# Optimization experiments

Hardware: AMD Instinct MI355X
Metric: run time of the kernel (lower is better)

## Reference

```python
import jax, jax.numpy as jnp
import numpy as np

PATCH = (9, 7, 5, 3)
DIM = 64
HEAD_DIM = 64
HEADS = 8
HIDDEN = 8
DEPTH = 4
SCALE = (HEAD_DIM / HEADS) ** (-0.5)  # per-head dim = 8
EPS = 1e-5


def setup_inputs() -> dict:
    key = jax.random.key(0)
    ks = jax.random.split(key, 8)
    B = 4096
    x = jax.random.normal(ks[0], (B, PATCH[0] * PATCH[0], DIM), dtype=jnp.float32)
    w_qkv = jax.random.normal(ks[1], (DEPTH, DIM, 3 * HEAD_DIM), dtype=jnp.float32) * 0.05
    b_qkv = jnp.zeros((DEPTH, 3 * HEAD_DIM), dtype=jnp.float32)
    w_o = jax.random.normal(ks[2], (DEPTH, HEAD_DIM, DIM), dtype=jnp.float32) * 0.05
    b_o = jnp.zeros((DEPTH, DIM), dtype=jnp.float32)
    ln1_g = jnp.ones((DEPTH, DIM), dtype=jnp.float32)
    ln1_b = jnp.zeros((DEPTH, DIM), dtype=jnp.float32)
    ln2_g = jnp.ones((DEPTH, DIM), dtype=jnp.float32)
    ln2_b = jnp.zeros((DEPTH, DIM), dtype=jnp.float32)
    w1 = jax.random.normal(ks[3], (DEPTH, DIM, HIDDEN), dtype=jnp.float32) * 0.05
    b1 = jnp.zeros((DEPTH, HIDDEN), dtype=jnp.float32)
    w2 = jax.random.normal(ks[4], (DEPTH, HIDDEN, DIM), dtype=jnp.float32) * 0.05
    b2 = jnp.zeros((DEPTH, DIM), dtype=jnp.float32)
    return {"x": x, "w_qkv": w_qkv, "b_qkv": b_qkv, "w_o": w_o, "b_o": b_o,
            "ln1_g": ln1_g, "ln1_b": ln1_b, "ln2_g": ln2_g, "ln2_b": ln2_b,
            "w1": w1, "b1": b1, "w2": w2, "b2": b2}


def _layernorm(x, g, b):
    m = jnp.mean(x, axis=-1, keepdims=True)
    v = jnp.mean(jnp.square(x - m), axis=-1, keepdims=True)
    return (x - m) * jax.lax.rsqrt(v + EPS) * g + b


def reference(x, w_qkv, b_qkv, w_o, b_o, ln1_g, ln1_b, ln2_g, ln2_b, w1, b1, w2, b2):
    B = x.shape[0]
    for i in range(DEPTH):
        n = x.shape[1]
        # --- attention block (Residual(Layernorm(Encoder))) ---
        y = _layernorm(x, ln1_g[i], ln1_b[i])
        qkv = y @ w_qkv[i] + b_qkv[i]                       # [B, n, 3*HEAD_DIM]
        q, k, v = jnp.split(qkv, 3, axis=-1)
        dh = HEAD_DIM // HEADS                              # 8
        q = q.reshape(B, n, HEADS, dh)
        k = k.reshape(B, n, HEADS, dh)
        v = v.reshape(B, n, HEADS, dh)
        dots = jnp.einsum('bihd,bjhd->bhij', q, k) * SCALE  # [B, H, n, n]
        attn = jax.nn.softmax(dots, axis=-1)
        out = jnp.einsum('bhij,bjhd->bihd', attn, v).reshape(B, n, HEAD_DIM)
        out = out @ w_o[i] + b_o[i]
        x = x + out                                         # dropout = identity (eval)
        # --- feedforward block ---
        y = _layernorm(x, ln2_g[i], ln2_b[i])
        h = jax.nn.gelu(y @ w1[i] + b1[i], approximate=False)
        x = x + h @ w2[i] + b2[i]
        # --- spatial pooling / rearrange ---
        p = PATCH[i]
        xg = x.reshape(B, p, p, DIM)                        # 'b (h w) d -> b h w d'
        if i != DEPTH - 1:
            xg = xg[:, 1:-1, 1:-1, :]                       # crop pool_size=1
            x = xg.reshape(B, (p - 2) * (p - 2), DIM)
        else:
            x = jnp.transpose(xg, (0, 3, 1, 2))             # 'b h w d -> b d h w'
    return x  # [B, 64, 3, 3]
```

## Files before the change

kernel.cpp:

```cpp
#include <hip/hip_runtime.h>
#include <hip/hip_bf16.h>
#include <math.h>

#define NT 512

typedef __attribute__((ext_vector_type(8))) short short8v;
typedef __attribute__((ext_vector_type(4))) short short4v;
typedef __attribute__((ext_vector_type(4))) float f32x4;
typedef __attribute__((ext_vector_type(2))) unsigned uint2v;
typedef __attribute__((ext_vector_type(4))) unsigned uint4v;

__device__ __forceinline__ unsigned short f2bf(float x) {
    unsigned u = __float_as_uint(x);
    unsigned r = ((u >> 16) & 1u) + 0x7FFFu;
    return (unsigned short)((u + r) >> 16);
}
__device__ __forceinline__ unsigned pk2(float a, float b) {
    __hip_bfloat162 h = __float22bfloat162_rn(make_float2(a, b));
    unsigned r;
    __builtin_memcpy(&r, &h, sizeof(r));
    return r;
}
__device__ __forceinline__ short bf1(float a) {
    __hip_bfloat16 h = __float2bfloat16(a);
    short r;
    __builtin_memcpy(&r, &h, sizeof(r));
    return r;
}
__device__ __forceinline__ float exp2fast(float x) {
#if __has_builtin(__builtin_amdgcn_exp2f)
    return __builtin_amdgcn_exp2f(x);
#else
    return exp2f(x);
#endif
}
__device__ __forceinline__ float gelu_f(float x) {
    float x3 = x * x * x;
    float e = exp2fast(-2.3022079f * x - 0.1029432f * x3);
    return x / (1.0f + e);
}
__device__ __forceinline__ f32x4 mfma32(short8v a, short8v b, f32x4 c) {
    return __builtin_amdgcn_mfma_f32_16x16x32_bf16(a, b, c, 0, 0, 0);
}

template<int M>
__device__ __forceinline__ float sum_tree(const f32x4* a) {
    float p[M];
    #pragma unroll
    for (int i = 0; i < M; ++i)
        p[i] = (a[i][0] + a[i][1]) + (a[i][2] + a[i][3]);
    #pragma unroll
    for (int s = 1; s < M; s *= 2)
        #pragma unroll
        for (int i = 0; i + s < M; i += 2 * s) p[i] += p[i + s];
    return p[0];
}
template<int M>
__device__ __forceinline__ void stats_tree(const f32x4* v, float& s1o, float& s2o) {
    float a[M], b[M];
    #pragma unroll
    for (int i = 0; i < M; ++i) {
        a[i] = (v[i][0] + v[i][1]) + (v[i][2] + v[i][3]);
        float q0 = v[i][0] * v[i][0], q1 = v[i][1] * v[i][1];
        float q2 = v[i][2] * v[i][2], q3 = v[i][3] * v[i][3];
        b[i] = (q0 + q1) + (q2 + q3);
    }
    #pragma unroll
    for (int s = 1; s < M; s *= 2)
        #pragma unroll
        for (int i = 0; i + s < M; i += 2 * s) { a[i] += a[i + s]; b[i] += b[i + s]; }
    s1o = a[0]; s2o = b[0];
}

#define WS_WO 49152
#define WS_W1 65536
#define WS_W2 69632
#define WS_TOT 71680

__global__ __launch_bounds__(256) void prep_kernel(
    const float* __restrict__ w_qkv, const float* __restrict__ w_o,
    const float* __restrict__ w1, const float* __restrict__ w2,
    short* __restrict__ ws)
{
    int idx = blockIdx.x * 256 + threadIdx.x;
    if (idx < WS_WO) {
        int l = idx / 12288, r = idx % 12288, c = r >> 6, d = r & 63;
        ws[idx] = (short)f2bf(w_qkv[l * 12288 + d * 192 + c]);
    } else if (idx < WS_W1) {
        int k = idx - WS_WO; int l = k / 4096, r = k % 4096, c = r >> 6, d = r & 63;
        ws[idx] = (short)f2bf(w_o[l * 4096 + d * 64 + c]);
    } else if (idx < WS_W2) {
        int k = idx - WS_W1; int l = k / 1024, r = k % 1024, j = r >> 6, d = r & 63;
        ws[idx] = (j < 8) ? (short)f2bf(w1[l * 512 + d * 8 + j]) : (short)0;
    } else if (idx < WS_TOT) {
        int k = idx - WS_W2; int l = k / 512, r = k % 512, c = r >> 3, j = r & 7;
        ws[idx] = (short)f2bf(w2[l * 512 + j * 64 + c]);
    }
}

template<int N, int P, int L, bool FIRST, bool LAST>
__device__ __forceinline__ void layer_fn(
    float* __restrict__ xs, short* __restrict__ y, short* __restrict__ vb,
    short* __restrict__ qbf, short* __restrict__ kbf,
    const short* __restrict__ ws,
    const float* __restrict__ b_qkv, const float* __restrict__ b_o,
    const float* __restrict__ ln1_g, const float* __restrict__ ln1_b,
    const float* __restrict__ ln2_g, const float* __restrict__ ln2_b,
    const float* __restrict__ b1,    const float* __restrict__ b2,
    float* __restrict__ out, int b, int t)
{
    constexpr int Mt = (N + 15) / 16;
    constexpr float SCL2E = 0.51010905835f;
    const int wv = t >> 6, l = t & 63, lr = l & 15, lq = l >> 4;
    short8v zero8 = {};
    f32x4 zero4 = {0.f, 0.f, 0.f, 0.f};

    if (FIRST) {
        if (t < 64 * Mt) {
            const int token = t >> 2, part = t & 3, d0 = part * 16;
            short* yrow = y + token * 72 + d0;
            if (token < N) {
                const int row = (token / P + L) * 9 + token % P + L;
                const float* xr = xs + row * 68 + d0;
                f32x4 v[4];
                #pragma unroll
                for (int k = 0; k < 4; ++k) v[k] = *(const f32x4*)(xr + 4 * k);
                float s1, s2;
                stats_tree<4>(v, s1, s2);
                s1 += __shfl_xor(s1, 1); s2 += __shfl_xor(s2, 1);
                s1 += __shfl_xor(s1, 2); s2 += __shfl_xor(s2, 2);
                const float m = s1 * 0.015625f;
                const float r = rsqrtf(s2 * 0.015625f - m * m + 1e-5f);
                uint4v w0, w1v;
                #pragma unroll
                for (int k = 0; k < 4; ++k) {
                    f32x4 g  = *(const f32x4*)&ln1_g[L * 64 + d0 + 4 * k];
                    f32x4 bb = *(const f32x4*)&ln1_b[L * 64 + d0 + 4 * k];
                    unsigned p0 = pk2((v[k][0]-m)*r*g[0]+bb[0], (v[k][1]-m)*r*g[1]+bb[1]);
                    unsigned p1 = pk2((v[k][2]-m)*r*g[2]+bb[2], (v[k][3]-m)*r*g[3]+bb[3]);
                    if (k == 0) { w0.x = p0; w0.y = p1; }
                    else if (k == 1) { w0.z = p0; w0.w = p1; }
                    else if (k == 2) { w1v.x = p0; w1v.y = p1; }
                    else { w1v.z = p0; w1v.w = p1; }
                }
                *(uint4v*)yrow = w0;
                *(uint4v*)(yrow + 8) = w1v;
            } else {
                uint4v z = {};
                *(uint4v*)yrow = z;
                *(uint4v*)(yrow + 8) = z;
            }
        }
        __syncthreads();
    }

    {
        const short* wqL = ws + L * 12288;
        for (int u = wv; u < Mt * 12; u += 8) {
            const int mt = u / 12, ct = u - mt * 12;
            const short* yr = &y[(16 * mt + lr) * 72 + lq * 8];
            short8v y0 = *(const short8v*)yr, y1 = *(const short8v*)(yr + 32);
            const short* wr = &wqL[(16 * ct + lr) * 64 + lq * 8];
            short8v w0 = *(const short8v*)wr, w1 = *(const short8v*)(wr + 32);
            if (ct < 8) {
                f32x4 acc = mfma32(w0, y0, zero4);
                acc = mfma32(w1, y1, acc);
                f32x4 bq = *(const f32x4*)&b_qkv[L * 192 + 16 * ct + lq * 4];
                const int i = 16 * mt + lr;
                if (ct < 4) {
                    unsigned p0 = pk2((acc[0]+bq[0])*SCL2E, (acc[1]+bq[1])*SCL2E);
                    unsigned p1 = pk2((acc[2]+bq[2])*SCL2E, (acc[3]+bq[3])*SCL2E);
                    unsigned* dst = (unsigned*)&qbf[i * 72 + 16 * ct + lq * 4];
                    dst[0] = p0; dst[1] = p1;
                } else {
                    unsigned p0 = pk2(acc[0]+bq[0], acc[1]+bq[1]);
                    unsigned p1 = pk2(acc[2]+bq[2], acc[3]+bq[3]);
                    unsigned* dst = (unsigned*)&kbf[i * 72 + 16 * (ct - 4) + lq * 4];
                    dst[0] = p0; dst[1] = p1;
                }
            } else {
                f32x4 acc = mfma32(y0, w0, zero4);
                acc = mfma32(y1, w1, acc);
                const int cv = 16 * (ct - 8) + lr;
                const float bias = b_qkv[L * 192 + 128 + cv];
                unsigned p0 = pk2(acc[0]+bias, acc[1]+bias);
                unsigned p1 = pk2(acc[2]+bias, acc[3]+bias);
                unsigned* dst = (unsigned*)&vb[cv * 104 + 16 * mt + lq * 4];
                dst[0] = p0; dst[1] = p1;
            }
        }
    }
    __syncthreads();

    {
        const int h = wv, hh = wv >> 1;
        short8v kf[Mt];
        #pragma unroll
        for (int jt = 0; jt < Mt; ++jt)
            kf[jt] = (l < 16) ? *(const short8v*)&kbf[(16 * jt + lr) * 72 + h * 8] : zero8;
#if __has_builtin(__builtin_amdgcn_mfma_f32_16x16x16bf16_1k)
        short4v vf[Mt];
        #pragma unroll
        for (int jt = 0; jt < Mt; ++jt)
            vf[jt] = *(const short4v*)&vb[(16 * hh + lr) * 104 + 16 * jt + lq * 4];
#else
        constexpr int KS2 = (Mt + 1) / 2;
        short8v vf8[KS2];
        #pragma unroll
        for (int ks = 0; ks < KS2; ++ks)
            vf8[ks] = *(const short8v*)&vb[(16 * hh + lr) * 104 + 32 * ks + lq * 8];
#endif
        for (int mt = 0; mt < Mt; ++mt) {
            short8v bq = (l < 16) ? *(const short8v*)&qbf[(16 * mt + lr) * 72 + h * 8] : zero8;
            f32x4 acc[Mt];
            #pragma unroll
            for (int jt = 0; jt < Mt; ++jt) acc[jt] = mfma32(kf[jt], bq, zero4);
            #pragma unroll
            for (int jt = 0; jt < Mt; ++jt) {
                #pragma unroll
                for (int rg = 0; rg < 4; ++rg) {
                    float e = exp2fast(acc[jt][rg]);
                    if (jt == Mt - 1) {
                        const int j = 16 * jt + lq * 4 + rg;
                        e = (j < N) ? e : 0.f;
                    }
                    acc[jt][rg] = e;
                }
            }
            float psum = sum_tree<Mt>(acc);
            float den = psum + __shfl_xor(psum, 16);
            den += __shfl_xor(den, 32);
            const float dinv = 1.0f / den;
            unsigned pkk[Mt][2];
            #pragma unroll
            for (int jt = 0; jt < Mt; ++jt) {
                pkk[jt][0] = pk2(acc[jt][0], acc[jt][1]);
                pkk[jt][1] = pk2(acc[jt][2], acc[jt][3]);
            }
            f32x4 po0 = zero4, po1 = zero4;
#if __has_builtin(__builtin_amdgcn_mfma_f32_16x16x16bf16_1k)
            #pragma unroll
            for (int jt = 0; jt < Mt; ++jt) {
                uint2v pw; pw.x = pkk[jt][0]; pw.y = pkk[jt][1];
                short4v bv = __builtin_bit_cast(short4v, pw);
                if (jt & 1) po1 = __builtin_amdgcn_mfma_f32_16x16x16bf16_1k(vf[jt], bv, po1, 0, 0, 0);
                else        po0 = __builtin_amdgcn_mfma_f32_16x16x16bf16_1k(vf[jt], bv, po0, 0, 0, 0);
            }
#else
            #pragma unroll
            for (int ks = 0; ks < KS2; ++ks) {
                const int t1ok = (2 * ks + 1) < Mt;
                unsigned pA0 = pkk[2 * ks][0], pA1 = pkk[2 * ks][1];
                unsigned pB0 = t1ok ? pkk[2 * ks + 1][0] : 0u;
                unsigned pB1 = t1ok ? pkk[2 * ks + 1][1] : 0u;
                int i01 = ((((lq & 1) * 2) * 16) + lr) * 4;
                int i23 = ((((lq & 1) * 2 + 1) * 16) + lr) * 4;
                unsigned w0a = (unsigned)__builtin_amdgcn_ds_bpermute(i01, (int)pA0);
                unsigned w0b = (unsigned)__builtin_amdgcn_ds_bpermute(i01, (int)pB0);
                unsigned w1a = (unsigned)__builtin_amdgcn_ds_bpermute(i01, (int)pA1);
                unsigned w1b = (unsigned)__builtin_amdgcn_ds_bpermute(i01, (int)pB1);
                unsigned w2a = (unsigned)__builtin_amdgcn_ds_bpermute(i23, (int)pA0);
                unsigned w2b = (unsigned)__builtin_amdgcn_ds_bpermute(i23, (int)pB0);
                unsigned w3a = (unsigned)__builtin_amdgcn_ds_bpermute(i23, (int)pA1);
                unsigned w3b = (unsigned)__builtin_amdgcn_ds_bpermute(i23, (int)pB1);
                uint4v wv4;
                wv4.x = (lq >> 1) ? w0b : w0a;
                wv4.y = (lq >> 1) ? w1b : w1a;
                wv4.z = (lq >> 1) ? w2b : w2a;
                wv4.w = (lq >> 1) ? w3b : w3a;
                short8v bv = __builtin_bit_cast(short8v, wv4);
                po0 = mfma32(vf8[ks], bv, po0);
            }
#endif
            if ((lq >> 1) == (h & 1)) {
                const int i = 16 * mt + lr;
                if (i < N) {
                    unsigned q0 = pk2((po0[0]+po1[0])*dinv, (po0[1]+po1[1])*dinv);
                    unsigned q1 = pk2((po0[2]+po1[2])*dinv, (po0[3]+po1[3])*dinv);
                    unsigned* dst = (unsigned*)&y[i * 72 + h * 8 + (lq & 1) * 4];
                    dst[0] = q0; dst[1] = q1;
                }
            }
        }
    }
    __syncthreads();

    {
        short* hb = qbf;
        if (wv < Mt) {
            const int mt = wv;
            const int i = 16 * mt + lr;
            const bool iok = (i < N);
            const int xrow = iok ? (i / P + L) * 9 + (i % P) + L : 0;
            float* xp = xs + xrow * 68;
            const short* yr = &y[i * 72 + lq * 8];
            short8v y0 = *(const short8v*)yr;
            short8v y1 = *(const short8v*)(yr + 32);
            const short* woL = ws + WS_WO + L * 4096;
            f32x4 xv[4];
            #pragma unroll
            for (int ct = 0; ct < 4; ++ct) {
                const short* wr = &woL[(16 * ct + lr) * 64 + lq * 8];
                f32x4 acc = mfma32(*(const short8v*)wr, y0, zero4);
                acc = mfma32(*(const short8v*)(wr + 32), y1, acc);
                f32x4 bo = *(const f32x4*)&b_o[L * 64 + 16 * ct + 4 * lq];
                f32x4 xc = zero4;
                if (iok) xc = *(const f32x4*)(xp + 16 * ct + 4 * lq);
                #pragma unroll
                for (int rg = 0; rg < 4; ++rg) xc[rg] += acc[rg] + bo[rg];
                xv[ct] = xc;
            }
            float s1, s2;
            stats_tree<4>(xv, s1, s2);
            s1 += __shfl_xor(s1, 16); s2 += __shfl_xor(s2, 16);
            s1 += __shfl_xor(s1, 32); s2 += __shfl_xor(s2, 32);
            const float m = s1 * 0.015625f;
            const float r = rsqrtf(s2 * 0.015625f - m * m + 1e-5f);
            unsigned* ybw = (unsigned*)&y[i * 72];
            #pragma unroll
            for (int ct = 0; ct < 4; ++ct) {
                f32x4 g  = *(const f32x4*)&ln2_g[L * 64 + 16 * ct + 4 * lq];
                f32x4 bb = *(const f32x4*)&ln2_b[L * 64 + 16 * ct + 4 * lq];
                ybw[8 * ct + 2 * lq]     = pk2((xv[ct][0]-m)*r*g[0]+bb[0],
                                               (xv[ct][1]-m)*r*g[1]+bb[1]);
                ybw[8 * ct + 2 * lq + 1] = pk2((xv[ct][2]-m)*r*g[2]+bb[2],
                                               (xv[ct][3]-m)*r*g[3]+bb[3]);
            }
            uint4v ua0 = *(const uint4v*)(ybw + 4 * lq);
            uint4v ua1 = *(const uint4v*)(ybw + 16 + 4 * lq);
            const short* w1L = ws + WS_W1 + L * 1024;
            short8v a10 = __builtin_bit_cast(short8v, ua0);
            short8v a11 = __builtin_bit_cast(short8v, ua1);
            short8v b10 = *(const short8v*)&w1L[lr * 64 + lq * 8];
            short8v b11 = *(const short8v*)&w1L[lr * 64 + lq * 8 + 32];
            f32x4 hA = mfma32(a10, b10, zero4);
            hA = mfma32(a11, b11, hA);
            if (lr < 8) {
                const float bg = b1[L * 8 + lr];
                #pragma unroll
                for (int rg = 0; rg < 4; ++rg)
                    hb[(16 * mt + 4 * lq + rg) * 8 + lr] = bf1(gelu_f(hA[rg] + bg));
            }
            short8v hbf = (lq == 0) ? *(const short8v*)&hb[(16 * mt + lr) * 8] : zero8;
            const short* w2L = ws + WS_W2 + L * 512;
            f32x4 xf[4];
            #pragma unroll
            for (int ct = 0; ct < 4; ++ct) {
                short8v a2 = (lq == 0) ? *(const short8v*)&w2L[(16 * ct + lr) * 8] : zero8;
                f32x4 dacc = mfma32(a2, hbf, zero4);
                f32x4 b2v = *(const f32x4*)&b2[L * 64 + 16 * ct + 4 * lq];
                #pragma unroll
                for (int rg = 0; rg < 4; ++rg) xf[ct][rg] = xv[ct][rg] + dacc[rg] + b2v[rg];
                if (iok) *(f32x4*)(xp + 16 * ct + 4 * lq) = xf[ct];
            }
            if (!LAST) {
                float t1, t2;
                stats_tree<4>(xf, t1, t2);
                t1 += __shfl_xor(t1, 16); t2 += __shfl_xor(t2, 16);
                t1 += __shfl_xor(t1, 32); t2 += __shfl_xor(t2, 32);
                const float mn = t1 * 0.015625f;
                const float rn = rsqrtf(t2 * 0.015625f - mn * mn + 1e-5f);
                const int r_ = i / P, c_ = i % P;
                const bool vok = iok && r_ >= 1 && r_ <= P - 2 && c_ >= 1 && c_ <= P - 2;
                if (vok) {
                    const int j = (r_ - 1) * (P - 2) + (c_ - 1);
                    unsigned* yw = (unsigned*)&vb[j * 72];
                    #pragma unroll
                    for (int ct = 0; ct < 4; ++ct) {
                        f32x4 g  = *(const f32x4*)&ln1_g[(L + 1) * 64 + 16 * ct + 4 * lq];
                        f32x4 bb = *(const f32x4*)&ln1_b[(L + 1) * 64 + 16 * ct + 4 * lq];
                        yw[8 * ct + 2 * lq]     = pk2((xf[ct][0]-mn)*rn*g[0]+bb[0],
                                                      (xf[ct][1]-mn)*rn*g[1]+bb[1]);
                        yw[8 * ct + 2 * lq + 1] = pk2((xf[ct][2]-mn)*rn*g[2]+bb[2],
                                                      (xf[ct][3]-mn)*rn*g[3]+bb[3]);
                    }
                }
            }
        } else if (!LAST && wv == Mt) {
            constexpr int Pn = P - 2, Nn = Pn * Pn, Mtn = (Nn + 15) / 16;
            constexpr int PadU = (16 * Mtn - Nn) * 36;
            unsigned* zb = (unsigned*)(vb + Nn * 72);
            for (int z = l; z < PadU; z += 64) zb[z] = 0;
        }
    }
    __syncthreads();

    if (LAST) {
        for (int idx = t; idx < 576; idx += NT) {
            const int d = idx / 9, rc = idx % 9;
            const int row = (rc / 3 + 3) * 9 + rc % 3 + 3;
            out[(size_t)b * 576 + idx] = xs[row * 68 + d];
        }
    }
}

__global__ __launch_bounds__(NT, 4) void vit_kernel(
    const float* __restrict__ x_in, const short* __restrict__ ws,
    const float* __restrict__ b_qkv, const float* __restrict__ b_o,
    const float* __restrict__ ln1_g, const float* __restrict__ ln1_b,
    const float* __restrict__ ln2_g, const float* __restrict__ ln2_b,
    const float* __restrict__ b1,    const float* __restrict__ b2,
    float* __restrict__ out)
{
    __shared__ __align__(16) float xs[81 * 68];
    __shared__ __align__(16) short ybf[96 * 72];
    __shared__ __align__(16) short vbuf[64 * 104];
    __shared__ __align__(16) short qbf[96 * 72];
    __shared__ __align__(16) short kbf[96 * 72];

    const int b = blockIdx.x;
    const int t = threadIdx.x;

    for (int idx = t; idx < 64 * 104; idx += NT) vbuf[idx] = 0;

    const float* xin = x_in + (size_t)b * 5184;
    for (int q4 = t; q4 < 1296; q4 += NT) {
        const int i = q4 >> 4, dq = q4 & 15;
        *(f32x4*)&xs[i * 68 + dq * 4] = *(const f32x4*)&xin[i * 64 + dq * 4];
    }
    __syncthreads();

    layer_fn<81, 9, 0, true,  false>(xs, ybf,  vbuf, qbf, kbf, ws, b_qkv, b_o,
                                     ln1_g, ln1_b, ln2_g, ln2_b, b1, b2, out, b, t);
    layer_fn<49, 7, 1, false, false>(xs, vbuf, ybf,  qbf, kbf, ws, b_qkv, b_o,
                                     ln1_g, ln1_b, ln2_g, ln2_b, b1, b2, out, b, t);
    layer_fn<25, 5, 2, false, false>(xs, ybf,  vbuf, qbf, kbf, ws, b_qkv, b_o,
                                     ln1_g, ln1_b, ln2_g, ln2_b, b1, b2, out, b, t);
    layer_fn<9,  3, 3, false, true >(xs, vbuf, ybf,  qbf, kbf, ws, b_qkv, b_o,
                                     ln1_g, ln1_b, ln2_g, ln2_b, b1, b2, out, b, t);
}

extern "C" void kernel_launch(void* const* d_in, const int* in_sizes, int n_in,
                              void* d_out, int out_size, void* d_ws, size_t ws_size,
                              hipStream_t stream) {
    (void)n_in; (void)out_size; (void)ws_size;
    const float* x     = (const float*)d_in[0];
    const float* w_qkv = (const float*)d_in[1];
    const float* b_qkv = (const float*)d_in[2];
    const float* w_o   = (const float*)d_in[3];
    const float* b_o   = (const float*)d_in[4];
    const float* ln1_g = (const float*)d_in[5];
    const float* ln1_b = (const float*)d_in[6];
    const float* ln2_g = (const float*)d_in[7];
    const float* ln2_b = (const float*)d_in[8];
    const float* w1    = (const float*)d_in[9];
    const float* b1    = (const float*)d_in[10];
    const float* w2    = (const float*)d_in[11];
    const float* b2    = (const float*)d_in[12];
    short* ws = (short*)d_ws;

    prep_kernel<<<dim3((WS_TOT + 255) / 256), dim3(256), 0, stream>>>(w_qkv, w_o, w1, w2, ws);

    int B = in_sizes[0] / (81 * 64);
    vit_kernel<<<dim3(B), dim3(NT), 0, stream>>>(
        x, ws, b_qkv, b_o, ln1_g, ln1_b, ln2_g, ln2_b, b1, b2, (float*)d_out);
}
```

Before: 377.2 us.

## Software-pipeline attention score MFMAs across row tiles and use fast reciprocal

```diff
diff --git a/kernel.cpp b/kernel.cpp
--- a/kernel.cpp
+++ b/kernel.cpp
@@ -34,10 +34,17 @@
     return exp2f(x);
 #endif
 }
+__device__ __forceinline__ float rcpfast(float x) {
+#if __has_builtin(__builtin_amdgcn_rcpf)
+    return __builtin_amdgcn_rcpf(x);
+#else
+    return 1.0f / x;
+#endif
+}
 __device__ __forceinline__ float gelu_f(float x) {
     float x3 = x * x * x;
     float e = exp2fast(-2.3022079f * x - 0.1029432f * x3);
-    return x / (1.0f + e);
+    return x * rcpfast(1.0f + e);
 }
 __device__ __forceinline__ f32x4 mfma32(short8v a, short8v b, f32x4 c) {
     return __builtin_amdgcn_mfma_f32_16x16x32_bf16(a, b, c, 0, 0, 0);
@@ -210,11 +217,12 @@
         for (int ks = 0; ks < KS2; ++ks)
             vf8[ks] = *(const short8v*)&vb[(16 * hh + lr) * 104 + 32 * ks + lq * 8];
 #endif
-        for (int mt = 0; mt < Mt; ++mt) {
-            short8v bq = (l < 16) ? *(const short8v*)&qbf[(16 * mt + lr) * 72 + h * 8] : zero8;
-            f32x4 acc[Mt];
+        auto SCORES = [&](int mt2, f32x4 (&acc)[Mt]) {
+            short8v bq = (l < 16) ? *(const short8v*)&qbf[(16 * mt2 + lr) * 72 + h * 8] : zero8;
             #pragma unroll
             for (int jt = 0; jt < Mt; ++jt) acc[jt] = mfma32(kf[jt], bq, zero4);
+        };
+        auto FINISH = [&](int mt2, f32x4 (&acc)[Mt]) {
             #pragma unroll
             for (int jt = 0; jt < Mt; ++jt) {
                 #pragma unroll
@@ -230,7 +238,7 @@
             float psum = sum_tree<Mt>(acc);
             float den = psum + __shfl_xor(psum, 16);
             den += __shfl_xor(den, 32);
-            const float dinv = 1.0f / den;
+            const float dinv = rcpfast(den);
             unsigned pkk[Mt][2];
             #pragma unroll
             for (int jt = 0; jt < Mt; ++jt) {
@@ -273,13 +281,25 @@
             }
 #endif
             if ((lq >> 1) == (h & 1)) {
-                const int i = 16 * mt + lr;
+                const int i = 16 * mt2 + lr;
                 if (i < N) {
                     unsigned q0 = pk2((po0[0]+po1[0])*dinv, (po0[1]+po1[1])*dinv);
                     unsigned q1 = pk2((po0[2]+po1[2])*dinv, (po0[3]+po1[3])*dinv);
                     unsigned* dst = (unsigned*)&y[i * 72 + h * 8 + (lq & 1) * 4];
                     dst[0] = q0; dst[1] = q1;
                 }
+            }
+        };
+        f32x4 sA[Mt], sB[Mt];
+        SCORES(0, sA);
+        #pragma unroll
+        for (int mt = 0; mt < Mt; ++mt) {
+            if (mt & 1) {
+                if (mt + 1 < Mt) SCORES(mt + 1, sA);
+                FINISH(mt, sB);
+            } else {
+                if (mt + 1 < Mt) SCORES(mt + 1, sB);
+                FINISH(mt, sA);
             }
         }
     }
```

New measurement: 372.7 us (median of 2 runs). Within noise of the previous version (-1.2%).

## Fuse QKV projection into per-head attention with register-resident fragments

Applied to the files above, without the earlier changes.

```diff
diff --git a/kernel.cpp b/kernel.cpp
--- a/kernel.cpp
+++ b/kernel.cpp
@@ -34,27 +34,25 @@
     return exp2f(x);
 #endif
 }
+__device__ __forceinline__ float rcpfast(float x) {
+#if __has_builtin(__builtin_amdgcn_rcpf)
+    return __builtin_amdgcn_rcpf(x);
+#else
+    return 1.0f / x;
+#endif
+}
 __device__ __forceinline__ float gelu_f(float x) {
     float x3 = x * x * x;
     float e = exp2fast(-2.3022079f * x - 0.1029432f * x3);
-    return x / (1.0f + e);
+    return x * rcpfast(1.0f + e);
 }
 __device__ __forceinline__ f32x4 mfma32(short8v a, short8v b, f32x4 c) {
     return __builtin_amdgcn_mfma_f32_16x16x32_bf16(a, b, c, 0, 0, 0);
 }
-
-template<int M>
-__device__ __forceinline__ float sum_tree(const f32x4* a) {
-    float p[M];
-    #pragma unroll
-    for (int i = 0; i < M; ++i)
-        p[i] = (a[i][0] + a[i][1]) + (a[i][2] + a[i][3]);
-    #pragma unroll
-    for (int s = 1; s < M; s *= 2)
-        #pragma unroll
-        for (int i = 0; i + s < M; i += 2 * s) p[i] += p[i + s];
-    return p[0];
-}
+__device__ __forceinline__ f32x4 mfma16(short4v a, short4v b, f32x4 c) {
+    return __builtin_amdgcn_mfma_f32_16x16x16bf16_1k(a, b, c, 0, 0, 0);
+}
+
 template<int M>
 __device__ __forceinline__ void stats_tree(const f32x4* v, float& s1o, float& s2o) {
     float a[M], b[M];
@@ -100,9 +98,8 @@
 
 template<int N, int P, int L, bool FIRST, bool LAST>
 __device__ __forceinline__ void layer_fn(
-    float* __restrict__ xs, short* __restrict__ y, short* __restrict__ vb,
-    short* __restrict__ qbf, short* __restrict__ kbf,
-    const short* __restrict__ ws,
+    float* __restrict__ xs, short* __restrict__ ybuf, short* __restrict__ abuf,
+    short* __restrict__ hb, const short* __restrict__ ws,
     const float* __restrict__ b_qkv, const float* __restrict__ b_o,
     const float* __restrict__ ln1_g, const float* __restrict__ ln1_b,
     const float* __restrict__ ln2_g, const float* __restrict__ ln2_b,
@@ -118,7 +115,7 @@
     if (FIRST) {
         if (t < 64 * Mt) {
             const int token = t >> 2, part = t & 3, d0 = part * 16;
-            short* yrow = y + token * 72 + d0;
+            short* yrow = ybuf + token * 72 + d0;
             if (token < N) {
                 const int row = (token / P + L) * 9 + token % P + L;
                 const float* xr = xs + row * 68 + d0;
@@ -155,129 +152,102 @@
     }
 
     {
+        const int h = wv, a = h & 1, ct = h >> 1;
+        const int srcl = lr + 32 * a + (l & 16);
         const short* wqL = ws + L * 12288;
-        for (int u = wv; u < Mt * 12; u += 8) {
-            const int mt = u / 12, ct = u - mt * 12;
-            const short* yr = &y[(16 * mt + lr) * 72 + lq * 8];
-            short8v y0 = *(const short8v*)yr, y1 = *(const short8v*)(yr + 32);
-            const short* wr = &wqL[(16 * ct + lr) * 64 + lq * 8];
-            short8v w0 = *(const short8v*)wr, w1 = *(const short8v*)(wr + 32);
-            if (ct < 8) {
-                f32x4 acc = mfma32(w0, y0, zero4);
-                acc = mfma32(w1, y1, acc);
-                f32x4 bq = *(const f32x4*)&b_qkv[L * 192 + 16 * ct + lq * 4];
-                const int i = 16 * mt + lr;
-                if (ct < 4) {
-                    unsigned p0 = pk2((acc[0]+bq[0])*SCL2E, (acc[1]+bq[1])*SCL2E);
-                    unsigned p1 = pk2((acc[2]+bq[2])*SCL2E, (acc[3]+bq[3])*SCL2E);
-                    unsigned* dst = (unsigned*)&qbf[i * 72 + 16 * ct + lq * 4];
-                    dst[0] = p0; dst[1] = p1;
-                } else {
-                    unsigned p0 = pk2(acc[0]+bq[0], acc[1]+bq[1]);
-                    unsigned p1 = pk2(acc[2]+bq[2], acc[3]+bq[3]);
-                    unsigned* dst = (unsigned*)&kbf[i * 72 + 16 * (ct - 4) + lq * 4];
-                    dst[0] = p0; dst[1] = p1;
+
+        short4v vf[Mt];
+        {
+            const short* wvr = &wqL[(128 + 16 * ct + lr) * 64 + lq * 8];
+            short8v wv0 = *(const short8v*)wvr, wv1 = *(const short8v*)(wvr + 32);
+            const float vb = b_qkv[L * 192 + 128 + 16 * ct + lr];
+            #pragma unroll
+            for (int mt = 0; mt < Mt; ++mt) {
+                const short* yr = &ybuf[(16 * mt + lr) * 72 + lq * 8];
+                short8v y0 = *(const short8v*)yr, y1 = *(const short8v*)(yr + 32);
+                f32x4 acc = mfma32(y0, wv0, zero4);
+                acc = mfma32(y1, wv1, acc);
+                uint2v u;
+                u.x = pk2(acc[0] + vb, acc[1] + vb);
+                u.y = pk2(acc[2] + vb, acc[3] + vb);
+                vf[mt] = __builtin_bit_cast(short4v, u);
+            }
+        }
+        uint2v kf[Mt];
+        {
+            const short* wkr = &wqL[(64 + 16 * ct + lr) * 64 + lq * 8];
+            short8v wk0 = *(const short8v*)wkr, wk1 = *(const short8v*)(wkr + 32);
+            f32x4 kb = *(const f32x4*)&b_qkv[L * 192 + 64 + 16 * ct + lq * 4];
+            #pragma unroll
+            for (int mt = 0; mt < Mt; ++mt) {
+                const short* yr = &ybuf[(16 * mt + lr) * 72 + lq * 8];
+                short8v y0 = *(const short8v*)yr, y1 = *(const short8v*)(yr + 32);
+                f32x4 acc = mfma32(wk0, y0, zero4);
+                acc = mfma32(wk1, y1, acc);
+                unsigned ka = pk2(acc[0] + kb[0], acc[1] + kb[1]);
+                unsigned kc = pk2(acc[2] + kb[2], acc[3] + kb[3]);
+                unsigned u0 = (unsigned)__shfl((int)ka, srcl);
+                unsigned u1 = (unsigned)__shfl((int)kc, srcl);
+                uint2v kv; kv.x = (l < 32) ? u0 : 0u; kv.y = (l < 32) ? u1 : 0u;
+                kf[mt] = kv;
+            }
+        }
+        uint2v qf[Mt];
+        {
+            const short* wqr = &wqL[(16 * ct + lr) * 64 + lq * 8];
+            short8v wq0 = *(const short8v*)wqr, wq1 = *(const short8v*)(wqr + 32);
+            f32x4 qb = *(const f32x4*)&b_qkv[L * 192 + 16 * ct + lq * 4];
+            #pragma unroll
+            for (int mt = 0; mt < Mt; ++mt) {
+                const short* yr = &ybuf[(16 * mt + lr) * 72 + lq * 8];
+                short8v y0 = *(const short8v*)yr, y1 = *(const short8v*)(yr + 32);
+                f32x4 acc = mfma32(wq0, y0, zero4);
+                acc = mfma32(wq1, y1, acc);
+                unsigned qa = pk2((acc[0] + qb[0]) * SCL2E, (acc[1] + qb[1]) * SCL2E);
+                unsigned qc = pk2((acc[2] + qb[2]) * SCL2E, (acc[3] + qb[3]) * SCL2E);
+                unsigned u0 = (unsigned)__shfl((int)qa, srcl);
+                unsigned u1 = (unsigned)__shfl((int)qc, srcl);
+                uint2v qv; qv.x = (l < 32) ? u0 : 0u; qv.y = (l < 32) ? u1 : 0u;
+                qf[mt] = qv;
+            }
+        }
+        for (int mt = 0; mt < Mt; ++mt) {
+            short4v qv = __builtin_bit_cast(short4v, qf[mt]);
+            uint2v pkk[Mt];
+            float psA = 0.f, psB = 0.f;
+            #pragma unroll
+            for (int jt = 0; jt < Mt; ++jt) {
+                f32x4 s = mfma16(__builtin_bit_cast(short4v, kf[jt]), qv, zero4);
+                float e0 = exp2fast(s[0]), e1 = exp2fast(s[1]);
+                float e2 = exp2fast(s[2]), e3 = exp2fast(s[3]);
+                if (jt == Mt - 1) {
+                    const int j0 = 16 * jt + lq * 4;
+                    e0 = (j0 + 0 < N) ? e0 : 0.f;
+                    e1 = (j0 + 1 < N) ? e1 : 0.f;
+                    e2 = (j0 + 2 < N) ? e2 : 0.f;
+                    e3 = (j0 + 3 < N) ? e3 : 0.f;
                 }
-            } else {
-                f32x4 acc = mfma32(y0, w0, zero4);
-                acc = mfma32(y1, w1, acc);
-                const int cv = 16 * (ct - 8) + lr;
-                const float bias = b_qkv[L * 192 + 128 + cv];
-                unsigned p0 = pk2(acc[0]+bias, acc[1]+bias);
-                unsigned p1 = pk2(acc[2]+bias, acc[3]+bias);
-                unsigned* dst = (unsigned*)&vb[cv * 104 + 16 * mt + lq * 4];
-                dst[0] = p0; dst[1] = p1;
-            }
-        }
-    }
-    __syncthreads();
-
-    {
-        const int h = wv, hh = wv >> 1;
-        short8v kf[Mt];
-        #pragma unroll
-        for (int jt = 0; jt < Mt; ++jt)
-            kf[jt] = (l < 16) ? *(const short8v*)&kbf[(16 * jt + lr) * 72 + h * 8] : zero8;
-#if __has_builtin(__builtin_amdgcn_mfma_f32_16x16x16bf16_1k)
-        short4v vf[Mt];
-        #pragma unroll
-        for (int jt = 0; jt < Mt; ++jt)
-            vf[jt] = *(const short4v*)&vb[(16 * hh + lr) * 104 + 16 * jt + lq * 4];
-#else
-        constexpr int KS2 = (Mt + 1) / 2;
-        short8v vf8[KS2];
-        #pragma unroll
-        for (int ks = 0; ks < KS2; ++ks)
-            vf8[ks] = *(const short8v*)&vb[(16 * hh + lr) * 104 + 32 * ks + lq * 8];
-#endif
-        for (int mt = 0; mt < Mt; ++mt) {
-            short8v bq = (l < 16) ? *(const short8v*)&qbf[(16 * mt + lr) * 72 + h * 8] : zero8;
-            f32x4 acc[Mt];
-            #pragma unroll
-            for (int jt = 0; jt < Mt; ++jt) acc[jt] = mfma32(kf[jt], bq, zero4);
-            #pragma unroll
-            for (int jt = 0; jt < Mt; ++jt) {
-                #pragma unroll
-                for (int rg = 0; rg < 4; ++rg) {
-                    float e = exp2fast(acc[jt][rg]);
-                    if (jt == Mt - 1) {
-                        const int j = 16 * jt + lq * 4 + rg;
-                        e = (j < N) ? e : 0.f;
-                    }
-                    acc[jt][rg] = e;
-                }
-            }
-            float psum = sum_tree<Mt>(acc);
+                psA += e0 + e1; psB += e2 + e3;
+                uint2v pv; pv.x = pk2(e0, e1); pv.y = pk2(e2, e3);
+                pkk[jt] = pv;
+            }
+            float psum = psA + psB;
             float den = psum + __shfl_xor(psum, 16);
             den += __shfl_xor(den, 32);
-            const float dinv = 1.0f / den;
-            unsigned pkk[Mt][2];
+            const float dinv = rcpfast(den);
+            f32x4 po0 = zero4, po1 = zero4;
             #pragma unroll
             for (int jt = 0; jt < Mt; ++jt) {
-                pkk[jt][0] = pk2(acc[jt][0], acc[jt][1]);
-                pkk[jt][1] = pk2(acc[jt][2], acc[jt][3]);
-            }
-            f32x4 po0 = zero4, po1 = zero4;
-#if __has_builtin(__builtin_amdgcn_mfma_f32_16x16x16bf16_1k)
-            #pragma unroll
-            for (int jt = 0; jt < Mt; ++jt) {
-                uint2v pw; pw.x = pkk[jt][0]; pw.y = pkk[jt][1];
-                short4v bv = __builtin_bit_cast(short4v, pw);
-                if (jt & 1) po1 = __builtin_amdgcn_mfma_f32_16x16x16bf16_1k(vf[jt], bv, po1, 0, 0, 0);
-                else        po0 = __builtin_amdgcn_mfma_f32_16x16x16bf16_1k(vf[jt], bv, po0, 0, 0, 0);
-            }
-#else
-            #pragma unroll
-            for (int ks = 0; ks < KS2; ++ks) {
-                const int t1ok = (2 * ks + 1) < Mt;
-                unsigned pA0 = pkk[2 * ks][0], pA1 = pkk[2 * ks][1];
-                unsigned pB0 = t1ok ? pkk[2 * ks + 1][0] : 0u;
-                unsigned pB1 = t1ok ? pkk[2 * ks + 1][1] : 0u;
-                int i01 = ((((lq & 1) * 2) * 16) + lr) * 4;
-                int i23 = ((((lq & 1) * 2 + 1) * 16) + lr) * 4;
-                unsigned w0a = (unsigned)__builtin_amdgcn_ds_bpermute(i01, (int)pA0);
-                unsigned w0b = (unsigned)__builtin_amdgcn_ds_bpermute(i01, (int)pB0);
-                unsigned w1a = (unsigned)__builtin_amdgcn_ds_bpermute(i01, (int)pA1);
-                unsigned w1b = (unsigned)__builtin_amdgcn_ds_bpermute(i01, (int)pB1);
-                unsigned w2a = (unsigned)__builtin_amdgcn_ds_bpermute(i23, (int)pA0);
-                unsigned w2b = (unsigned)__builtin_amdgcn_ds_bpermute(i23, (int)pB0);
-                unsigned w3a = (unsigned)__builtin_amdgcn_ds_bpermute(i23, (int)pA1);
-                unsigned w3b = (unsigned)__builtin_amdgcn_ds_bpermute(i23, (int)pB1);
-                uint4v wv4;
-                wv4.x = (lq >> 1) ? w0b : w0a;
-                wv4.y = (lq >> 1) ? w1b : w1a;
-                wv4.z = (lq >> 1) ? w2b : w2a;
-                wv4.w = (lq >> 1) ? w3b : w3a;
-                short8v bv = __builtin_bit_cast(short8v, wv4);
-                po0 = mfma32(vf8[ks], bv, po0);
-            }
-#endif
-            if ((lq >> 1) == (h & 1)) {
+                short4v bv = __builtin_bit_cast(short4v, pkk[jt]);
+                if (jt & 1) po1 = mfma16(vf[jt], bv, po1);
+                else        po0 = mfma16(vf[jt], bv, po0);
+            }
+            if ((lq >> 1) == a) {
                 const int i = 16 * mt + lr;
                 if (i < N) {
-                    unsigned q0 = pk2((po0[0]+po1[0])*dinv, (po0[1]+po1[1])*dinv);
-                    unsigned q1 = pk2((po0[2]+po1[2])*dinv, (po0[3]+po1[3])*dinv);
-                    unsigned* dst = (unsigned*)&y[i * 72 + h * 8 + (lq & 1) * 4];
+                    unsigned q0 = pk2((po0[0] + po1[0]) * dinv, (po0[1] + po1[1]) * dinv);
+                    unsigned q1 = pk2((po0[2] + po1[2]) * dinv, (po0[3] + po1[3]) * dinv);
+                    unsigned* dst = (unsigned*)&abuf[i * 72 + h * 8 + (lq & 1) * 4];
                     dst[0] = q0; dst[1] = q1;
                 }
             }
@@ -286,29 +256,28 @@
     __syncthreads();
 
     {
-        short* hb = qbf;
         if (wv < Mt) {
             const int mt = wv;
             const int i = 16 * mt + lr;
             const bool iok = (i < N);
             const int xrow = iok ? (i / P + L) * 9 + (i % P) + L : 0;
             float* xp = xs + xrow * 68;
-            const short* yr = &y[i * 72 + lq * 8];
+            const short* yr = &abuf[i * 72 + lq * 8];
             short8v y0 = *(const short8v*)yr;
             short8v y1 = *(const short8v*)(yr + 32);
             const short* woL = ws + WS_WO + L * 4096;
             f32x4 xv[4];
             #pragma unroll
-            for (int ct = 0; ct < 4; ++ct) {
-                const short* wr = &woL[(16 * ct + lr) * 64 + lq * 8];
+            for (int ctp = 0; ctp < 4; ++ctp) {
+                const short* wr = &woL[(16 * ctp + lr) * 64 + lq * 8];
                 f32x4 acc = mfma32(*(const short8v*)wr, y0, zero4);
                 acc = mfma32(*(const short8v*)(wr + 32), y1, acc);
-                f32x4 bo = *(const f32x4*)&b_o[L * 64 + 16 * ct + 4 * lq];
+                f32x4 bo = *(const f32x4*)&b_o[L * 64 + 16 * ctp + 4 * lq];
                 f32x4 xc = zero4;
-                if (iok) xc = *(const f32x4*)(xp + 16 * ct + 4 * lq);
+                if (iok) xc = *(const f32x4*)(xp + 16 * ctp + 4 * lq);
                 #pragma unroll
                 for (int rg = 0; rg < 4; ++rg) xc[rg] += acc[rg] + bo[rg];
-                xv[ct] = xc;
+                xv[ctp] = xc;
             }
             float s1, s2;
             stats_tree<4>(xv, s1, s2);
@@ -316,18 +285,18 @@
             s1 += __shfl_xor(s1, 32); s2 += __shfl_xor(s2, 32);
             const float m = s1 * 0.015625f;
             const float r = rsqrtf(s2 * 0.015625f - m * m + 1e-5f);
-            unsigned* ybw = (unsigned*)&y[i * 72];
-            #pragma unroll
-            for (int ct = 0; ct < 4; ++ct) {
-                f32x4 g  = *(const f32x4*)&ln2_g[L * 64 + 16 * ct + 4 * lq];
-                f32x4 bb = *(const f32x4*)&ln2_b[L * 64 + 16 * ct + 4 * lq];
-                ybw[8 * ct + 2 * lq]     = pk2((xv[ct][0]-m)*r*g[0]+bb[0],
-                                               (xv[ct][1]-m)*r*g[1]+bb[1]);
-                ybw[8 * ct + 2 * lq + 1] = pk2((xv[ct][2]-m)*r*g[2]+bb[2],
-                                               (xv[ct][3]-m)*r*g[3]+bb[3]);
-            }
-            uint4v ua0 = *(const uint4v*)(ybw + 4 * lq);
-            uint4v ua1 = *(const uint4v*)(ybw + 16 + 4 * lq);
+            unsigned* abw = (unsigned*)&abuf[i * 72];
+            #pragma unroll
+            for (int ctp = 0; ctp < 4; ++ctp) {
+                f32x4 g  = *(const f32x4*)&ln2_g[L * 64 + 16 * ctp + 4 * lq];
+                f32x4 bb = *(const f32x4*)&ln2_b[L * 64 + 16 * ctp + 4 * lq];
+                abw[8 * ctp + 2 * lq]     = pk2((xv[ctp][0]-m)*r*g[0]+bb[0],
+                                                (xv[ctp][1]-m)*r*g[1]+bb[1]);
+                abw[8 * ctp + 2 * lq + 1] = pk2((xv[ctp][2]-m)*r*g[2]+bb[2],
+                                                (xv[ctp][3]-m)*r*g[3]+bb[3]);
+            }
+            uint4v ua0 = *(const uint4v*)(abw + 4 * lq);
+            uint4v ua1 = *(const uint4v*)(abw + 16 + 4 * lq);
             const short* w1L = ws + WS_W1 + L * 1024;
             short8v a10 = __builtin_bit_cast(short8v, ua0);
             short8v a11 = __builtin_bit_cast(short8v, ua1);
@@ -345,13 +314,13 @@
             const short* w2L = ws + WS_W2 + L * 512;
             f32x4 xf[4];
             #pragma unroll
-            for (int ct = 0; ct < 4; ++ct) {
-                short8v a2 = (lq == 0) ? *(const short8v*)&w2L[(16 * ct + lr) * 8] : zero8;
+            for (int ctp = 0; ctp < 4; ++ctp) {
+                short8v a2 = (lq == 0) ? *(const short8v*)&w2L[(16 * ctp + lr) * 8] : zero8;
                 f32x4 dacc = mfma32(a2, hbf, zero4);
-                f32x4 b2v = *(const f32x4*)&b2[L * 64 + 16 * ct + 4 * lq];
+                f32x4 b2v = *(const f32x4*)&b2[L * 64 + 16 * ctp + 4 * lq];
                 #pragma unroll
-                for (int rg = 0; rg < 4; ++rg) xf[ct][rg] = xv[ct][rg] + dacc[rg] + b2v[rg];
-                if (iok) *(f32x4*)(xp + 16 * ct + 4 * lq) = xf[ct];
+                for (int rg = 0; rg < 4; ++rg) xf[ctp][rg] = xv[ctp][rg] + dacc[rg] + b2v[rg];
+                if (iok) *(f32x4*)(xp + 16 * ctp + 4 * lq) = xf[ctp];
             }
             if (!LAST) {
                 float t1, t2;
@@ -364,22 +333,22 @@
                 const bool vok = iok && r_ >= 1 && r_ <= P - 2 && c_ >= 1 && c_ <= P - 2;
                 if (vok) {
                     const int j = (r_ - 1) * (P - 2) + (c_ - 1);
-                    unsigned* yw = (unsigned*)&vb[j * 72];
+                    unsigned* yw = (unsigned*)&ybuf[j * 72];
                     #pragma unroll
-                    for (int ct = 0; ct < 4; ++ct) {
-                        f32x4 g  = *(const f32x4*)&ln1_g[(L + 1) * 64 + 16 * ct + 4 * lq];
-                        f32x4 bb = *(const f32x4*)&ln1_b[(L + 1) * 64 + 16 * ct + 4 * lq];
-                        yw[8 * ct + 2 * lq]     = pk2((xf[ct][0]-mn)*rn*g[0]+bb[0],
-                                                      (xf[ct][1]-mn)*rn*g[1]+bb[1]);
-                        yw[8 * ct + 2 * lq + 1] = pk2((xf[ct][2]-mn)*rn*g[2]+bb[2],
-                                                      (xf[ct][3]-mn)*rn*g[3]+bb[3]);
+                    for (int ctp = 0; ctp < 4; ++ctp) {
+                        f32x4 g  = *(const f32x4*)&ln1_g[(L + 1) * 64 + 16 * ctp + 4 * lq];
+                        f32x4 bb = *(const f32x4*)&ln1_b[(L + 1) * 64 + 16 * ctp + 4 * lq];
+                        yw[8 * ctp + 2 * lq]     = pk2((xf[ctp][0]-mn)*rn*g[0]+bb[0],
+                                                       (xf[ctp][1]-mn)*rn*g[1]+bb[1]);
+                        yw[8 * ctp + 2 * lq + 1] = pk2((xf[ctp][2]-mn)*rn*g[2]+bb[2],
+                                                       (xf[ctp][3]-mn)*rn*g[3]+bb[3]);
                     }
                 }
             }
         } else if (!LAST && wv == Mt) {
             constexpr int Pn = P - 2, Nn = Pn * Pn, Mtn = (Nn + 15) / 16;
             constexpr int PadU = (16 * Mtn - Nn) * 36;
-            unsigned* zb = (unsigned*)(vb + Nn * 72);
+            unsigned* zb = (unsigned*)(ybuf + Nn * 72);
             for (int z = l; z < PadU; z += 64) zb[z] = 0;
         }
     }
@@ -394,7 +363,7 @@
     }
 }
 
-__global__ __launch_bounds__(NT, 4) void vit_kernel(
+__global__ __launch_bounds__(NT, 8) void vit_kernel(
     const float* __restrict__ x_in, const short* __restrict__ ws,
     const float* __restrict__ b_qkv, const float* __restrict__ b_o,
     const float* __restrict__ ln1_g, const float* __restrict__ ln1_b,
@@ -403,15 +372,14 @@
     float* __restrict__ out)
 {
     __shared__ __align__(16) float xs[81 * 68];
-    __shared__ __align__(16) short ybf[96 * 72];
-    __shared__ __align__(16) short vbuf[64 * 104];
-    __shared__ __align__(16) short qbf[96 * 72];
-    __shared__ __align__(16) short kbf[96 * 72];
+    __shared__ __align__(16) short ybuf[96 * 72];
+    __shared__ __align__(16) short abuf[96 * 72];
+    __shared__ __align__(16) short hb[96 * 8];
 
     const int b = blockIdx.x;
     const int t = threadIdx.x;
 
-    for (int idx = t; idx < 64 * 104; idx += NT) vbuf[idx] = 0;
+    for (int idx = t; idx < 96 * 72; idx += NT) abuf[idx] = 0;
 
     const float* xin = x_in + (size_t)b * 5184;
     for (int q4 = t; q4 < 1296; q4 += NT) {
@@ -420,13 +388,13 @@
     }
     __syncthreads();
 
-    layer_fn<81, 9, 0, true,  false>(xs, ybf,  vbuf, qbf, kbf, ws, b_qkv, b_o,
+    layer_fn<81, 9, 0, true,  false>(xs, ybuf, abuf, hb, ws, b_qkv, b_o,
                                      ln1_g, ln1_b, ln2_g, ln2_b, b1, b2, out, b, t);
-    layer_fn<49, 7, 1, false, false>(xs, vbuf, ybf,  qbf, kbf, ws, b_qkv, b_o,
+    layer_fn<49, 7, 1, false, false>(xs, ybuf, abuf, hb, ws, b_qkv, b_o,
                                      ln1_g, ln1_b, ln2_g, ln2_b, b1, b2, out, b, t);
-    layer_fn<25, 5, 2, false, false>(xs, ybf,  vbuf, qbf, kbf, ws, b_qkv, b_o,
+    layer_fn<25, 5, 2, false, false>(xs, ybuf, abuf, hb, ws, b_qkv, b_o,
                                      ln1_g, ln1_b, ln2_g, ln2_b, b1, b2, out, b, t);
-    layer_fn<9,  3, 3, false, true >(xs, vbuf, ybf,  qbf, kbf, ws, b_qkv, b_o,
+    layer_fn<9,  3, 3, false, true >(xs, ybuf, abuf, hb, ws, b_qkv, b_o,
                                      ln1_g, ln1_b, ln2_g, ln2_b, b1, b2, out, b, t);
 }
 
```

Result: slower. 465.3 us (+23.4%).
